# Optimization experiments

Measured on AMD Instinct MI355X. Metric: run time of the kernel, lower is better.

Reference implementation:

```python
import jax, jax.numpy as jnp
import numpy as np

DT = 0.01
OMEGA_MAX = 100.0


def setup_inputs() -> dict:
    key = jax.random.key(0)
    ks = jax.random.split(key, 7)
    B, T, D, M = 4, 4096, 1024, 64
    N = 2 * M
    u = jax.random.normal(ks[0], (B, T, D), dtype=jnp.float32)
    W_omega = jax.random.normal(ks[1], (M, D), dtype=jnp.float32) * 0.02
    b_omega = jnp.ones((M,), dtype=jnp.float32)
    W_zeta = jax.random.normal(ks[2], (M, D), dtype=jnp.float32) * 0.02
    b_zeta = jnp.zeros((M,), dtype=jnp.float32)
    W_B = jax.random.normal(ks[3], (N, D), dtype=jnp.float32) * (0.1 / np.sqrt(D))
    b_B = jnp.zeros((N,), dtype=jnp.float32)
    C = jax.random.normal(ks[4], (D, N), dtype=jnp.float32) * 0.01
    D_mat = jax.random.normal(ks[5], (D, D), dtype=jnp.float32) * 0.01
    return dict(u=u, W_omega=W_omega, b_omega=b_omega, W_zeta=W_zeta,
                b_zeta=b_zeta, W_B=W_B, b_B=b_B, C=C, D_mat=D_mat)


def reference(u, W_omega, b_omega, W_zeta, b_zeta, W_B, b_B, C, D_mat):
    B, T, D = u.shape
    M = W_omega.shape[0]
    # Hoist all per-step linear projections into batched GEMMs (same math).
    omega = jax.nn.softplus(jnp.einsum('btd,md->btm', u, W_omega) + b_omega)
    omega = jnp.clip(omega, 1e-4, OMEGA_MAX)                      # (B,T,M)
    zeta = jax.nn.sigmoid(jnp.einsum('btd,md->btm', u, W_zeta) + b_zeta)
    A = omega * omega                                             # (B,T,M)
    S = 1.0 / (1.0 + (DT * DT) * A)                               # (B,T,M)
    d = 1.0 - zeta                                                # (B,T,M)
    F = jnp.einsum('btd,nd->btn', u, W_B) + b_B                   # (B,T,2M)

    def step(x, inp):
        A_t, S_t, d_t, F_t = inp                                  # (B,M)x3, (B,2M)
        z = x[:, :M]
        y = x[:, M:]
        z_new = d_t * (S_t * z - DT * A_t * S_t * y)
        y_new = d_t * (DT * S_t * z + S_t * y)
        x_new = jnp.concatenate([z_new, y_new], axis=-1) + F_t
        return x_new, x_new

    x0 = jnp.zeros((B, 2 * M), dtype=u.dtype)
    tm = lambda a: jnp.swapaxes(a, 0, 1)  # to time-major for scan
    _, xs = jax.lax.scan(step, x0, (tm(A), tm(S), tm(d), tm(F)))
    xs = jnp.swapaxes(xs, 0, 1)                                   # (B,T,2M)
    # Output projection: y_t = x_t C^T + u_t D^T
    y = jnp.einsum('btn,dn->btd', xs, C) + jnp.einsum('bte,de->btd', u, D_mat)
    return y
```

## Files before the change

### kernel.cpp

```cpp
#include <hip/hip_runtime.h>
#include <hip/hip_bf16.h>
#include <math.h>

#define DTC 0.01f

typedef __attribute__((ext_vector_type(8))) short short8;
typedef __attribute__((ext_vector_type(4))) float f32x4;
typedef unsigned short bf16raw;

__device__ __forceinline__ bf16raw f2bf(float f){
  union { unsigned u; float f; } v; v.f = f;
  unsigned r = v.u + 0x7FFF + ((v.u >> 16) & 1u);
  return (bf16raw)(r >> 16);
}

__device__ __forceinline__ short8 ld8f(const float* __restrict__ p){
  float4 a = *(const float4*)p;
  float4 b = *(const float4*)(p + 4);
  short8 r;
  r[0] = (short)f2bf(a.x); r[1] = (short)f2bf(a.y);
  r[2] = (short)f2bf(a.z); r[3] = (short)f2bf(a.w);
  r[4] = (short)f2bf(b.x); r[5] = (short)f2bf(b.y);
  r[6] = (short)f2bf(b.z); r[7] = (short)f2bf(b.w);
  return r;
}

template<int ITERS>
__device__ __forceinline__ void stage_async(const bf16raw* __restrict__ src, long ld,
                                            long row0, int k0, bf16raw* lds,
                                            int wave, int lane){
#pragma unroll
  for (int i = 0; i < ITERS; ++i){
    int r0 = (wave*ITERS + i) * 16;
    long row = row0 + r0 + (lane >> 2);
    const bf16raw* gp = src + row*ld + k0 + (lane & 3)*8;
    bf16raw* lp = lds + r0*32;
    __builtin_amdgcn_global_load_lds((const __attribute__((address_space(1))) void*)gp,
                                     (__attribute__((address_space(3))) void*)lp,
                                     16, 0, 0);
  }
}

template<int NI>
__device__ __forceinline__ void mma_tile(const bf16raw* Alds, const bf16raw* Blds,
                                         f32x4 acc[4][NI], int wm, int wn, int quad, int t16){
  short8 af[4], bfr[NI];
#pragma unroll
  for (int mi = 0; mi < 4; ++mi)
    af[mi] = *(const short8*)(Alds + (wm*64 + mi*16 + t16)*32 + quad*8);
#pragma unroll
  for (int ni = 0; ni < NI; ++ni)
    bfr[ni] = *(const short8*)(Blds + (wn*(NI*16) + ni*16 + t16)*32 + quad*8);
#pragma unroll
  for (int mi = 0; mi < 4; ++mi)
#pragma unroll
    for (int ni = 0; ni < NI; ++ni)
      acc[mi][ni] = __builtin_amdgcn_mfma_f32_16x16x32_bf16(af[mi], bfr[ni], acc[mi][ni], 0, 0, 0);
}

extern "C" __global__ void k_prep(const float* __restrict__ u,
    const float* __restrict__ Wom, const float* __restrict__ Wze,
    const float* __restrict__ WB, const float* __restrict__ Cm,
    const float* __restrict__ Dm, bf16raw* __restrict__ u_bf,
    bf16raw* __restrict__ Wcat, bf16raw* __restrict__ C_bf,
    bf16raw* __restrict__ Dm_bf){
  long g = (long)blockIdx.x * 256 + threadIdx.x;
  const float* src; bf16raw* dst; long o;
  if      (g < 2097152){ src = u;   dst = u_bf;          o = g; }
  else if (g < 2105344){ src = Wom; dst = Wcat;          o = g - 2097152; }
  else if (g < 2113536){ src = Wze; dst = Wcat + 65536;  o = g - 2105344; }
  else if (g < 2129920){ src = WB;  dst = Wcat + 131072; o = g - 2113536; }
  else if (g < 2146304){ src = Cm;  dst = C_bf;          o = g - 2129920; }
  else                 { src = Dm;  dst = Dm_bf;         o = g - 2146304; }
  *(short8*)(dst + o*8) = ld8f(src + o*8);
}

extern "C" __global__ __launch_bounds__(256) void k_gemm_p(
    const bf16raw* __restrict__ u_bf, const bf16raw* __restrict__ Wcat,
    float* __restrict__ P){
  __shared__ __align__(16) bf16raw Alds[2][128*32];
  __shared__ __align__(16) bf16raw Blds[2][128*32];
  int tid = threadIdx.x, wave = tid >> 6, lane = tid & 63;
  int quad = lane >> 4, t16 = lane & 15;
  int wm = wave >> 1, wn = wave & 1;
  int id  = blockIdx.y * gridDim.x + blockIdx.x;
  int sid = (id & 7) * 32 + (id >> 3);
  long row0 = (long)(sid >> 1) * 128;
  int  col0 = (sid & 1) * 128;
  f32x4 acc[4][4] = {};

  stage_async<2>(u_bf, 1024, row0, 0, Alds[0], wave, lane);
  stage_async<2>(Wcat, 1024, col0, 0, Blds[0], wave, lane);
  asm volatile("s_waitcnt vmcnt(0)" ::: "memory");
  __builtin_amdgcn_s_barrier();
  __builtin_amdgcn_sched_barrier(0);
  int cur = 0;
  for (int kt = 0; kt < 31; ++kt){
    stage_async<2>(u_bf, 1024, row0, (kt+1)*32, Alds[cur^1], wave, lane);
    stage_async<2>(Wcat, 1024, col0, (kt+1)*32, Blds[cur^1], wave, lane);
    __builtin_amdgcn_s_setprio(1);
    mma_tile<4>(Alds[cur], Blds[cur], acc, wm, wn, quad, t16);
    __builtin_amdgcn_s_setprio(0);
    asm volatile("s_waitcnt vmcnt(0)" ::: "memory");
    __builtin_amdgcn_s_barrier();
    __builtin_amdgcn_sched_barrier(0);
    cur ^= 1;
  }
  mma_tile<4>(Alds[cur], Blds[cur], acc, wm, wn, quad, t16);
#pragma unroll
  for (int mi = 0; mi < 4; ++mi)
#pragma unroll
    for (int ni = 0; ni < 4; ++ni)
#pragma unroll
      for (int r = 0; r < 4; ++r){
        long grow = row0 + wm*64 + mi*16 + quad*4 + r;
        int  gcol = col0 + wn*64 + ni*16 + t16;
        P[grow*256 + gcol] = acc[mi][ni][r];
      }
}

extern "C" __global__ __launch_bounds__(256, 2) void k_gemm_out(
    const bf16raw* __restrict__ Xs, const bf16raw* __restrict__ u_bf,
    const bf16raw* __restrict__ C_bf, const bf16raw* __restrict__ Dm_bf,
    float* __restrict__ out){
  __shared__ __align__(16) bf16raw Alds[2][128*32];
  __shared__ __align__(16) bf16raw Blds[2][256*32];
  int tid = threadIdx.x, wave = tid >> 6, lane = tid & 63;
  int quad = lane >> 4, t16 = lane & 15;
  int wm = wave >> 1, wn = wave & 1;
  int id  = blockIdx.y * gridDim.x + blockIdx.x;
  int sid = (id & 7) * 64 + (id >> 3);
  long row0 = (long)(sid >> 2) * 128;
  int  col0 = (sid & 3) * 256;
  f32x4 acc[4][8] = {};

  auto stage = [&](int s, int buf){
    if (s < 4){
      stage_async<2>(Xs,   128, row0, s*32, Alds[buf], wave, lane);
      stage_async<4>(C_bf, 128, col0, s*32, Blds[buf], wave, lane);
    } else {
      stage_async<2>(u_bf,  1024, row0, (s-4)*32, Alds[buf], wave, lane);
      stage_async<4>(Dm_bf, 1024, col0, (s-4)*32, Blds[buf], wave, lane);
    }
  };

  stage(0, 0);
  asm volatile("s_waitcnt vmcnt(0)" ::: "memory");
  __builtin_amdgcn_s_barrier();
  __builtin_amdgcn_sched_barrier(0);
  int cur = 0;
  for (int s = 0; s < 35; ++s){
    stage(s+1, cur^1);
    __builtin_amdgcn_s_setprio(1);
    mma_tile<8>(Alds[cur], Blds[cur], acc, wm, wn, quad, t16);
    __builtin_amdgcn_s_setprio(0);
    asm volatile("s_waitcnt vmcnt(0)" ::: "memory");
    __builtin_amdgcn_s_barrier();
    __builtin_amdgcn_sched_barrier(0);
    cur ^= 1;
  }
  mma_tile<8>(Alds[cur], Blds[cur], acc, wm, wn, quad, t16);
#pragma unroll
  for (int mi = 0; mi < 4; ++mi)
#pragma unroll
    for (int ni = 0; ni < 8; ++ni)
#pragma unroll
      for (int r = 0; r < 4; ++r){
        long grow = row0 + wm*64 + mi*16 + quad*4 + r;
        int  gcol = col0 + wn*128 + ni*16 + t16;
        out[grow*1024 + gcol] = acc[mi][ni][r];
      }
}

extern "C" __global__ __launch_bounds__(256) void k_scanA(
    const float* __restrict__ P, const float* __restrict__ b_om,
    const float* __restrict__ b_ze, const float* __restrict__ b_B,
    float4* __restrict__ Coef, float4* __restrict__ CM, float2* __restrict__ CV){
  int tid = threadIdx.x, c = blockIdx.x;
  int b = tid >> 6, m = tid & 63;
  float bo = b_om[m], bz = b_ze[m], bb0 = b_B[m], bb1 = b_B[64 + m];
  const float* row = P + ((size_t)b*4096 + c*16) * 256;
  float4* cf = Coef + ((size_t)b*4096 + c*16) * 64 + m;
  float m00=1.f, m01=0.f, m10=0.f, m11=0.f, vz=0.f, vy=0.f;
#pragma unroll 4
  for (int t = 0; t < 16; ++t){
    const float* r = row + t*256;
    float wo = r[m]       + bo;
    float wz = r[64 + m]  + bz;
    float fz = r[128 + m] + bb0;
    float fy = r[192 + m] + bb1;
    float sp = (wo > 20.f) ? wo : log1pf(expf(wo));
    float omega = fminf(fmaxf(sp, 1e-4f), 100.f);
    float A = omega * omega;
    float S = 1.f / (1.f + DTC*DTC*A);
    float zeta = 1.f / (1.f + expf(-wz));
    float p = (1.f - zeta) * S;
    float q = p * DTC * A;
    cf[t*64] = make_float4(p, q, fz, fy);
    float nvz = p*vz - q*vy + fz;
    float nvy = DTC*p*vz + p*vy + fy;
    vz = nvz; vy = nvy;
    float n00 = p*m00 - q*m10;
    float n01 = p*m01 - q*m11;
    float n10 = DTC*p*m00 + p*m10;
    float n11 = DTC*p*m01 + p*m11;
    m00=n00; m01=n01; m10=n10; m11=n11;
  }
  CM[c*256 + tid] = make_float4(m00, m01, m10, m11);
  CV[c*256 + tid] = make_float2(vz, vy);
}

extern "C" __global__ __launch_bounds__(256) void k_scanC(
    const float4* __restrict__ Coef, const float4* __restrict__ CM,
    const float2* __restrict__ CV, bf16raw* __restrict__ Xs){
  int tid = threadIdx.x, c = blockIdx.x;
  int b = tid >> 6, m = tid & 63;
  float xz = 0.f, xy = 0.f;
#pragma unroll 4
  for (int j = 0; j < c; ++j){
    float4 Mv = CM[j*256 + tid];
    float2 Vv = CV[j*256 + tid];
    float nz = Mv.x*xz + Mv.y*xy + Vv.x;
    float ny = Mv.z*xz + Mv.w*xy + Vv.y;
    xz = nz; xy = ny;
  }
  const float4* cf = Coef + ((size_t)b*4096 + c*16) * 64 + m;
  bf16raw* xp = Xs + ((size_t)b*4096 + c*16) * 128 + m;
#pragma unroll 4
  for (int t = 0; t < 16; ++t){
    float4 f = cf[t*64];
    float nz = f.x*xz - f.y*xy + f.z;
    float ny = DTC*f.x*xz + f.x*xy + f.w;
    xz = nz; xy = ny;
    xp[t*128]      = f2bf(xz);
    xp[t*128 + 64] = f2bf(xy);
  }
}

extern "C" void kernel_launch(void* const* d_in, const int* in_sizes, int n_in,
                              void* d_out, int out_size, void* d_ws, size_t ws_size,
                              hipStream_t stream){
  const float* u   = (const float*)d_in[0];
  const float* Wom = (const float*)d_in[1];
  const float* bom = (const float*)d_in[2];
  const float* Wze = (const float*)d_in[3];
  const float* bze = (const float*)d_in[4];
  const float* WB  = (const float*)d_in[5];
  const float* bB  = (const float*)d_in[6];
  const float* Cm  = (const float*)d_in[7];
  const float* Dm  = (const float*)d_in[8];
  float* out = (float*)d_out;

  char* ws = (char*)d_ws;
  size_t off = 0;
  bf16raw* u_bf  = (bf16raw*)(ws + off); off += (size_t)16777216*2;
  bf16raw* Wcat  = (bf16raw*)(ws + off); off += (size_t)262144*2;
  bf16raw* C_bf  = (bf16raw*)(ws + off); off += (size_t)131072*2;
  bf16raw* Dm_bf = (bf16raw*)(ws + off); off += (size_t)1048576*2;
  float*   P     = (float*)  (ws + off);
  bf16raw* Xs    = (bf16raw*)P;
  off += (size_t)16384*256*4;
  float4*  Coef  = (float4*) (ws + off); off += (size_t)16384*64*16;
  float4*  CMw   = (float4*) (ws + off); off += (size_t)256*256*16;
  float2*  CVw   = (float2*) (ws + off); off += (size_t)256*256*8;

  k_prep    <<<8896, 256, 0, stream>>>(u, Wom, Wze, WB, Cm, Dm, u_bf, Wcat, C_bf, Dm_bf);
  k_gemm_p  <<<dim3(2, 128), 256, 0, stream>>>(u_bf, Wcat, P);
  k_scanA   <<<256, 256, 0, stream>>>(P, bom, bze, bB, Coef, CMw, CVw);
  k_scanC   <<<256, 256, 0, stream>>>(Coef, CMw, CVw, Xs);
  k_gemm_out<<<dim3(4, 128), 256, 0, stream>>>(Xs, u_bf, C_bf, Dm_bf, out);
}
```

Measured before the change: 240.5 us.

## Swizzle LDS k-chunks and restructure GEMM loops to keep two tiles in flight

The global-to-LDS async loads now permute each row's 16-byte k-chunks with an XOR swizzle, and the MFMA fragment reads apply the matching XOR. This is meant to spread the LDS reads across banks. Both GEMM kernels now prefetch two stages up front and wait with partial vmcnt counts instead of vmcnt(0), so the next tile's loads stay outstanding while the current tile is computed. The change relies on the vmcnt thresholds matching the number of loads each stage issues; a wrong count would produce a data race.

```diff
diff --git a/kernel.cpp b/kernel.cpp
--- a/kernel.cpp
+++ b/kernel.cpp
@@ -29,11 +29,12 @@
 __device__ __forceinline__ void stage_async(const bf16raw* __restrict__ src, long ld,
                                             long row0, int k0, bf16raw* lds,
                                             int wave, int lane){
+  int kchunk = (lane & 3) ^ ((lane >> 3) & 3);
 #pragma unroll
   for (int i = 0; i < ITERS; ++i){
     int r0 = (wave*ITERS + i) * 16;
     long row = row0 + r0 + (lane >> 2);
-    const bf16raw* gp = src + row*ld + k0 + (lane & 3)*8;
+    const bf16raw* gp = src + row*ld + k0 + kchunk*8;
     bf16raw* lp = lds + r0*32;
     __builtin_amdgcn_global_load_lds((const __attribute__((address_space(1))) void*)gp,
                                      (__attribute__((address_space(3))) void*)lp,
@@ -45,12 +46,13 @@
 __device__ __forceinline__ void mma_tile(const bf16raw* Alds, const bf16raw* Blds,
                                          f32x4 acc[4][NI], int wm, int wn, int quad, int t16){
   short8 af[4], bfr[NI];
-#pragma unroll
-  for (int mi = 0; mi < 4; ++mi)
-    af[mi] = *(const short8*)(Alds + (wm*64 + mi*16 + t16)*32 + quad*8);
+  int sw = (quad ^ ((t16 >> 1) & 3)) * 8;
+#pragma unroll
+  for (int mi = 0; mi < 4; ++mi)
+    af[mi] = *(const short8*)(Alds + (wm*64 + mi*16 + t16)*32 + sw);
 #pragma unroll
   for (int ni = 0; ni < NI; ++ni)
-    bfr[ni] = *(const short8*)(Blds + (wn*(NI*16) + ni*16 + t16)*32 + quad*8);
+    bfr[ni] = *(const short8*)(Blds + (wn*(NI*16) + ni*16 + t16)*32 + sw);
 #pragma unroll
   for (int mi = 0; mi < 4; ++mi)
 #pragma unroll
@@ -89,24 +91,32 @@
   int  col0 = (sid & 1) * 128;
   f32x4 acc[4][4] = {};
 
-  stage_async<2>(u_bf, 1024, row0, 0, Alds[0], wave, lane);
-  stage_async<2>(Wcat, 1024, col0, 0, Blds[0], wave, lane);
+  auto stage = [&](int kt, int buf){
+    stage_async<2>(u_bf, 1024, row0, kt*32, Alds[buf], wave, lane);
+    stage_async<2>(Wcat, 1024, col0, kt*32, Blds[buf], wave, lane);
+  };
+
+  stage(0, 0);
+  stage(1, 1);
+  for (int kt = 0; kt < 30; ++kt){
+    asm volatile("s_waitcnt vmcnt(4)" ::: "memory");
+    __builtin_amdgcn_s_barrier();
+    __builtin_amdgcn_sched_barrier(0);
+    __builtin_amdgcn_s_setprio(1);
+    mma_tile<4>(Alds[kt & 1], Blds[kt & 1], acc, wm, wn, quad, t16);
+    __builtin_amdgcn_s_setprio(0);
+    __builtin_amdgcn_sched_barrier(0);
+    __builtin_amdgcn_s_barrier();
+    stage(kt + 2, kt & 1);
+  }
+  asm volatile("s_waitcnt vmcnt(4)" ::: "memory");
+  __builtin_amdgcn_s_barrier();
+  __builtin_amdgcn_sched_barrier(0);
+  mma_tile<4>(Alds[0], Blds[0], acc, wm, wn, quad, t16);
   asm volatile("s_waitcnt vmcnt(0)" ::: "memory");
   __builtin_amdgcn_s_barrier();
   __builtin_amdgcn_sched_barrier(0);
-  int cur = 0;
-  for (int kt = 0; kt < 31; ++kt){
-    stage_async<2>(u_bf, 1024, row0, (kt+1)*32, Alds[cur^1], wave, lane);
-    stage_async<2>(Wcat, 1024, col0, (kt+1)*32, Blds[cur^1], wave, lane);
-    __builtin_amdgcn_s_setprio(1);
-    mma_tile<4>(Alds[cur], Blds[cur], acc, wm, wn, quad, t16);
-    __builtin_amdgcn_s_setprio(0);
-    asm volatile("s_waitcnt vmcnt(0)" ::: "memory");
-    __builtin_amdgcn_s_barrier();
-    __builtin_amdgcn_sched_barrier(0);
-    cur ^= 1;
-  }
-  mma_tile<4>(Alds[cur], Blds[cur], acc, wm, wn, quad, t16);
+  mma_tile<4>(Alds[1], Blds[1], acc, wm, wn, quad, t16);
 #pragma unroll
   for (int mi = 0; mi < 4; ++mi)
 #pragma unroll
@@ -145,21 +155,26 @@
   };
 
   stage(0, 0);
+  stage(1, 1);
+  for (int s = 0; s < 34; ++s){
+    asm volatile("s_waitcnt vmcnt(6)" ::: "memory");
+    __builtin_amdgcn_s_barrier();
+    __builtin_amdgcn_sched_barrier(0);
+    __builtin_amdgcn_s_setprio(1);
+    mma_tile<8>(Alds[s & 1], Blds[s & 1], acc, wm, wn, quad, t16);
+    __builtin_amdgcn_s_setprio(0);
+    __builtin_amdgcn_sched_barrier(0);
+    __builtin_amdgcn_s_barrier();
+    stage(s + 2, s & 1);
+  }
+  asm volatile("s_waitcnt vmcnt(6)" ::: "memory");
+  __builtin_amdgcn_s_barrier();
+  __builtin_amdgcn_sched_barrier(0);
+  mma_tile<8>(Alds[0], Blds[0], acc, wm, wn, quad, t16);
   asm volatile("s_waitcnt vmcnt(0)" ::: "memory");
   __builtin_amdgcn_s_barrier();
   __builtin_amdgcn_sched_barrier(0);
-  int cur = 0;
-  for (int s = 0; s < 35; ++s){
-    stage(s+1, cur^1);
-    __builtin_amdgcn_s_setprio(1);
-    mma_tile<8>(Alds[cur], Blds[cur], acc, wm, wn, quad, t16);
-    __builtin_amdgcn_s_setprio(0);
-    asm volatile("s_waitcnt vmcnt(0)" ::: "memory");
-    __builtin_amdgcn_s_barrier();
-    __builtin_amdgcn_sched_barrier(0);
-    cur ^= 1;
-  }
-  mma_tile<8>(Alds[cur], Blds[cur], acc, wm, wn, quad, t16);
+  mma_tile<8>(Alds[1], Blds[1], acc, wm, wn, quad, t16);
 #pragma unroll
   for (int mi = 0; mi < 4; ++mi)
 #pragma unroll
```

Result: no change. 236.5 us (-1.7%).
